# Optimization experiments

Hardware: AMD Instinct MI355X
Metric: run time of the kernel (lower is better)

The kernel has to match this reference:

```python
import jax, jax.numpy as jnp
import numpy as np

H = 512          # hidden_size
SF = 4           # scale_factor
B, S, L = 16, 2048, 2

def setup_inputs() -> dict:
    key = jax.random.key(0)
    ks = jax.random.split(key, 9)
    return {
        "hidden": jax.random.normal(ks[0], (L, B, H * SF), dtype=jnp.float32),
        "encoder_outputs": jax.random.normal(ks[1], (B, S, H * SF), dtype=jnp.float32),
        "We": jax.random.normal(ks[2], (H, H * SF), dtype=jnp.float32) * 0.02,
        "be": jax.random.normal(ks[3], (H,), dtype=jnp.float32) * 0.02,
        "Wh": jax.random.normal(ks[4], (H, H * SF), dtype=jnp.float32) * 0.02,
        "bh": jax.random.normal(ks[5], (H,), dtype=jnp.float32) * 0.02,
        "Wa": jax.random.normal(ks[6], (H, 2 * H), dtype=jnp.float32) * 0.02,
        "ba": jax.random.normal(ks[7], (H,), dtype=jnp.float32) * 0.02,
        "v": jax.random.uniform(ks[8], (1, H), dtype=jnp.float32),
    }

def reference(hidden, encoder_outputs, We, be, Wh, bh, Wa, ba, v):
    # hidden[-1]: [B, 4H] -> [B, H]
    h = hidden[-1] @ Wh.T + bh
    # encoder_outputs: [B, S, 4H] -> [B, S, H]
    eo = jnp.einsum('bsf,hf->bsh', encoder_outputs, We) + be
    # concat([h broadcast to S, eo]) @ Wa.T == h @ Wa_h.T + eo @ Wa_e.T (split concat matmul)
    Wa_h, Wa_e = Wa[:, :H], Wa[:, H:]
    energy = jnp.tanh(h[:, None, :] @ Wa_h.T + jnp.einsum('bsh,kh->bsk', eo, Wa_e) + ba)  # [B,S,H]
    scores = jnp.einsum('bsh,h->bs', energy, v[0])           # [B,S]
    attn_weights = jax.nn.softmax(scores, axis=1)            # [B,S]
    context_vector = jnp.einsum('bs,bsh->bh', attn_weights, eo)  # [B,H]
    return (context_vector, attn_weights)
```

## Files before the change

kernel.cpp:

```cpp
#include <hip/hip_runtime.h>
#include <math.h>

#define HH 512
#define FF 2048
#define BB 16
#define SS 2048
#define MM 32768

using f32x4 = __attribute__((ext_vector_type(4))) float;
using s16x8 = __attribute__((ext_vector_type(8))) short;

struct __align__(8)  US4 { unsigned short x, y, z, w; };
struct __align__(16) US8 { unsigned short s[8]; };

__device__ __forceinline__ unsigned short f2bf(float f) {
  unsigned int u = __builtin_bit_cast(unsigned int, f);
  u += 0x7fffu + ((u >> 16) & 1u);
  return (unsigned short)(u >> 16);
}
__device__ __forceinline__ float bf2f(unsigned short u) {
  unsigned int x = ((unsigned int)u) << 16;
  return __builtin_bit_cast(float, x);
}
__device__ __forceinline__ void gload_lds16(const void* g, void* l) {
  __builtin_amdgcn_global_load_lds(
      (const __attribute__((address_space(1))) unsigned int*)g,
      (__attribute__((address_space(3))) unsigned int*)l, 16, 0, 0);
}

__global__ void k_conv(const float* __restrict__ We, const float* __restrict__ Wa,
                       unsigned short* __restrict__ OWe, unsigned short* __restrict__ OWa) {
  int bid = blockIdx.x, t = threadIdx.x;
  if (bid < 1024) {
    int idx = bid * 256 + t;
    f32x4 x = *(const f32x4*)(We + (size_t)idx * 4);
    US4 p{f2bf(x.x), f2bf(x.y), f2bf(x.z), f2bf(x.w)};
    *(US4*)(OWe + (size_t)idx * 4) = p;
  } else {
    int idx = (bid - 1024) * 256 + t;
    int k = idx >> 7, h4 = idx & 127;
    f32x4 x = *(const f32x4*)(Wa + (size_t)k * 1024 + 512 + h4 * 4);
    US4 p{f2bf(x.x), f2bf(x.y), f2bf(x.z), f2bf(x.w)};
    *(US4*)(OWa + (size_t)idx * 4) = p;
  }
}

__global__ void k_h(const float* __restrict__ hidden, const float* __restrict__ Wh,
                    const float* __restrict__ bh, float* __restrict__ h_ws) {
  int t = threadIdx.x, lane = t & 63, wid = t >> 6;
  int out = blockIdx.x * 4 + wid;
  int b = out >> 9, j = out & 511;
  const float* hr = hidden + (1) * BB * FF + b * FF;
  const float* wr = Wh + (size_t)j * FF;
  float a = 0.f;
#pragma unroll
  for (int i = 0; i < 8; ++i) {
    int o = i * 256 + lane * 4;
    f32x4 x = *(const f32x4*)(hr + o);
    f32x4 y = *(const f32x4*)(wr + o);
    a += x.x * y.x + x.y * y.y + x.z * y.z + x.w * y.w;
  }
#pragma unroll
  for (int m = 32; m; m >>= 1) a += __shfl_xor(a, m);
  if (lane == 0) h_ws[out] = a + bh[j];
}

__global__ void k_bb(const float* __restrict__ h_ws, const float* __restrict__ Wa,
                     const float* __restrict__ ba, float* __restrict__ bb_ws) {
  int t = threadIdx.x, lane = t & 63, wid = t >> 6;
  int out = blockIdx.x * 4 + wid;
  int b = out >> 9, k = out & 511;
  const float* hr = h_ws + b * HH;
  const float* wa = Wa + (size_t)k * 1024;
  float a = 0.f;
#pragma unroll
  for (int i = 0; i < 2; ++i) {
    int o = i * 256 + lane * 4;
    f32x4 x = *(const f32x4*)(hr + o);
    f32x4 y = *(const f32x4*)(wa + o);
    a += x.x * y.x + x.y * y.y + x.z * y.z + x.w * y.w;
  }
#pragma unroll
  for (int m = 32; m; m >>= 1) a += __shfl_xor(a, m);
  if (lane == 0) bb_ws[out] = a + ba[k];
}

__global__ __launch_bounds__(512, 4) void k_gemm1f(
    const float* __restrict__ enc, const unsigned short* __restrict__ Web,
    const float* __restrict__ be, const unsigned short* __restrict__ Waeb,
    const float* __restrict__ bbw, const float* __restrict__ vv,
    unsigned short* __restrict__ eo, float* __restrict__ sp) {
  __shared__ unsigned short smem[36864];
  unsigned short* As = smem;
  unsigned short* Bs = smem + 4096;
  const int t = threadIdx.x, lane = t & 63, wid = t >> 6;
  const int m0 = blockIdx.x * 64;
  const float* enc_m0 = enc + (size_t)m0 * FF;
  f32x4 acc[4][4] = {};

  f32x4 areg[2];
#pragma unroll
  for (int i = 0; i < 2; ++i) {
    int idx = i * 512 + t, row = idx >> 4, c4 = idx & 15;
    areg[i] = *(const f32x4*)(enc_m0 + (size_t)row * FF + c4 * 4);
  }

#pragma unroll 1
  for (int kt = 0; kt < FF; kt += 64) {
#pragma unroll
    for (int i = 0; i < 8; ++i) {
      int idx = i * 512 + t, row = idx >> 3, c = idx & 7, sc = c ^ (row & 7);
      gload_lds16(Web + (size_t)row * FF + kt + sc * 8, Bs + idx * 8);
    }
#pragma unroll
    for (int i = 0; i < 2; ++i) {
      int idx = i * 512 + t, row = idx >> 4, c4 = idx & 15;
      f32x4 x = areg[i];
      US4 p{f2bf(x.x), f2bf(x.y), f2bf(x.z), f2bf(x.w)};
      int byte = row * 128 + ((c4 * 8) ^ ((row & 7) << 4));
      *(US4*)((char*)As + byte) = p;
    }
    {
      int ktn = (kt + 64 < FF) ? kt + 64 : 0;
#pragma unroll
      for (int i = 0; i < 2; ++i) {
        int idx = i * 512 + t, row = idx >> 4, c4 = idx & 15;
        areg[i] = *(const f32x4*)(enc_m0 + (size_t)row * FF + ktn + c4 * 4);
      }
    }
    __syncthreads();
#pragma unroll
    for (int ks = 0; ks < 2; ++ks) {
      s16x8 af[4], bfr[4];
#pragma unroll
      for (int mi = 0; mi < 4; ++mi) {
        int row = mi * 16 + (lane & 15);
        int byte = row * 128 + (((ks * 64) + (lane >> 4) * 16) ^ ((row & 7) << 4));
        af[mi] = *(const s16x8*)((const char*)As + byte);
      }
#pragma unroll
      for (int ni = 0; ni < 4; ++ni) {
        int row = wid * 64 + ni * 16 + (lane & 15);
        int byte = row * 128 + (((ks * 64) + (lane >> 4) * 16) ^ ((row & 7) << 4));
        bfr[ni] = *(const s16x8*)((const char*)Bs + byte);
      }
#pragma unroll
      for (int mi = 0; mi < 4; ++mi)
#pragma unroll
        for (int ni = 0; ni < 4; ++ni)
          acc[mi][ni] = __builtin_amdgcn_mfma_f32_16x16x32_bf16(af[mi], bfr[ni], acc[mi][ni], 0, 0, 0);
    }
    __syncthreads();
  }

  unsigned short* Cs = smem + 4096;
#pragma unroll
  for (int ni = 0; ni < 4; ++ni) {
    int col = wid * 64 + ni * 16 + (lane & 15);
    float bev = be[col];
#pragma unroll
    for (int mi = 0; mi < 4; ++mi)
#pragma unroll
      for (int j = 0; j < 4; ++j) {
        int row = mi * 16 + (lane >> 4) * 4 + j;
        int byte = row * 1024 + ((col * 2) ^ ((row & 7) << 4));
        *(unsigned short*)((char*)Cs + byte) = f2bf(acc[mi][ni][j] + bev);
      }
  }
  __syncthreads();

#pragma unroll
  for (int i = 0; i < 8; ++i) {
    int idx = i * 512 + t, row = idx >> 6, c = idx & 63;
    int byte = row * 1024 + ((c * 16) ^ ((row & 7) << 4));
    *(US8*)(eo + (size_t)(m0 + row) * HH + c * 8) = *(const US8*)((const char*)Cs + byte);
  }

  f32x4 acc2[4][4] = {};
#pragma unroll 1
  for (int kt2 = 0; kt2 < HH; kt2 += 64) {
#pragma unroll
    for (int ks = 0; ks < 2; ++ks) {
      int k2 = kt2 + ks * 32 + (lane >> 4) * 8;
      s16x8 af[4], bfr[4];
#pragma unroll
      for (int mi = 0; mi < 4; ++mi) {
        int row = mi * 16 + (lane & 15);
        int byte = row * 1024 + ((k2 * 2) ^ ((row & 7) << 4));
        af[mi] = *(const s16x8*)((const char*)Cs + byte);
      }
#pragma unroll
      for (int ni = 0; ni < 4; ++ni) {
        int nrow = wid * 64 + ni * 16 + (lane & 15);
        bfr[ni] = *(const s16x8*)(Waeb + (size_t)nrow * HH + k2);
      }
#pragma unroll
      for (int mi = 0; mi < 4; ++mi)
#pragma unroll
        for (int ni = 0; ni < 4; ++ni)
          acc2[mi][ni] = __builtin_amdgcn_mfma_f32_16x16x32_bf16(af[mi], bfr[ni], acc2[mi][ni], 0, 0, 0);
    }
  }

  const int b = m0 >> 11;
  float vcol[4], bcol[4];
#pragma unroll
  for (int ni = 0; ni < 4; ++ni) {
    int col = wid * 64 + ni * 16 + (lane & 15);
    vcol[ni] = vv[col];
    bcol[ni] = bbw[b * HH + col];
  }
  float ps[4][4];
#pragma unroll
  for (int mi = 0; mi < 4; ++mi)
#pragma unroll
    for (int j = 0; j < 4; ++j) {
      float s = 0.f;
#pragma unroll
      for (int ni = 0; ni < 4; ++ni)
        s += tanhf(acc2[mi][ni][j] + bcol[ni]) * vcol[ni];
      ps[mi][j] = s;
    }
#pragma unroll
  for (int m = 1; m < 16; m <<= 1)
#pragma unroll
    for (int mi = 0; mi < 4; ++mi)
#pragma unroll
      for (int j = 0; j < 4; ++j) ps[mi][j] += __shfl_xor(ps[mi][j], m);
  float* red = (float*)smem;
  if ((lane & 15) == 0) {
#pragma unroll
    for (int mi = 0; mi < 4; ++mi)
#pragma unroll
      for (int j = 0; j < 4; ++j)
        red[wid * 64 + mi * 16 + (lane >> 4) * 4 + j] = ps[mi][j];
  }
  __syncthreads();
  if (t < 64) {
    float s = 0.f;
#pragma unroll
    for (int w = 0; w < 8; ++w) s += red[w * 64 + t];
    sp[m0 + t] = s;
  }
}

__global__ void k_softmax(const float* __restrict__ sp, float* __restrict__ attn) {
  const int b = blockIdx.x, t = threadIdx.x, lane = t & 63, wid = t >> 6;
  __shared__ float red[4];
  float vals[8], lmax = -3.0e38f;
#pragma unroll
  for (int i = 0; i < 8; ++i) {
    float x = sp[b * SS + t + i * 256];
    vals[i] = x;
    lmax = fmaxf(lmax, x);
  }
#pragma unroll
  for (int m = 32; m; m >>= 1) lmax = fmaxf(lmax, __shfl_xor(lmax, m));
  if (lane == 0) red[wid] = lmax;
  __syncthreads();
  lmax = fmaxf(fmaxf(red[0], red[1]), fmaxf(red[2], red[3]));
  __syncthreads();
  float lsum = 0.f;
#pragma unroll
  for (int i = 0; i < 8; ++i) {
    vals[i] = __expf(vals[i] - lmax);
    lsum += vals[i];
  }
#pragma unroll
  for (int m = 32; m; m >>= 1) lsum += __shfl_xor(lsum, m);
  if (lane == 0) red[wid] = lsum;
  __syncthreads();
  float inv = 1.0f / (red[0] + red[1] + red[2] + red[3]);
#pragma unroll
  for (int i = 0; i < 8; ++i) attn[b * SS + t + i * 256] = vals[i] * inv;
}

__global__ __launch_bounds__(512) void k_ctx1(const unsigned short* __restrict__ eo,
                                              const float* __restrict__ attn,
                                              float* __restrict__ cp) {
  __shared__ float red[8][512];
  const int b = blockIdx.x >> 4, ch = blockIdx.x & 15, t = threadIdx.x;
  const int tg = t & 63, sg = t >> 6;
  const float* aw = attn + b * SS + ch * 128;
  float acc[8] = {};
#pragma unroll 4
  for (int i = 0; i < 16; ++i) {
    int s = sg + i * 8;
    float w = aw[s];
    US8 vv8 = *(const US8*)(eo + (size_t)(b * SS + ch * 128 + s) * HH + tg * 8);
#pragma unroll
    for (int j = 0; j < 8; ++j) acc[j] += w * bf2f(vv8.s[j]);
  }
#pragma unroll
  for (int j = 0; j < 8; ++j) red[sg][tg * 8 + j] = acc[j];
  __syncthreads();
  float a = 0.f;
#pragma unroll
  for (int g = 0; g < 8; ++g) a += red[g][t];
  cp[(size_t)blockIdx.x * HH + t] = a;
}

__global__ void k_ctx2(const float* __restrict__ cp, float* __restrict__ ctx) {
  const int b = blockIdx.x, h = threadIdx.x;
  float a = 0.f;
#pragma unroll
  for (int c = 0; c < 16; ++c) a += cp[(size_t)(b * 16 + c) * HH + h];
  ctx[b * HH + h] = a;
}

extern "C" void kernel_launch(void* const* d_in, const int* in_sizes, int n_in,
                              void* d_out, int out_size, void* d_ws, size_t ws_size,
                              hipStream_t stream) {
  (void)in_sizes; (void)n_in; (void)out_size; (void)ws_size;
  const float* hidden = (const float*)d_in[0];
  const float* enc    = (const float*)d_in[1];
  const float* We     = (const float*)d_in[2];
  const float* be     = (const float*)d_in[3];
  const float* Wh     = (const float*)d_in[4];
  const float* bh     = (const float*)d_in[5];
  const float* Wa     = (const float*)d_in[6];
  const float* ba     = (const float*)d_in[7];
  const float* v      = (const float*)d_in[8];

  float* out  = (float*)d_out;
  float* ctx  = out;
  float* attn = out + BB * HH;

  char* ws = (char*)d_ws;
  unsigned short* Web  = (unsigned short*)ws;  ws += (size_t)HH * FF * 2;
  unsigned short* Waeb = (unsigned short*)ws;  ws += (size_t)HH * HH * 2;
  float* h_ws  = (float*)ws;                   ws += (size_t)BB * HH * 4;
  float* bb_ws = (float*)ws;                   ws += (size_t)BB * HH * 4;
  unsigned short* eo = (unsigned short*)ws;    ws += (size_t)MM * HH * 2;
  float* sp = (float*)ws;                      ws += (size_t)MM * 4;
  float* cp = (float*)ws;                      ws += (size_t)BB * 16 * HH * 4;

  k_conv<<<1280, 256, 0, stream>>>(We, Wa, Web, Waeb);
  k_h<<<2048, 256, 0, stream>>>(hidden, Wh, bh, h_ws);
  k_bb<<<2048, 256, 0, stream>>>(h_ws, Wa, ba, bb_ws);
  k_gemm1f<<<512, 512, 0, stream>>>(enc, Web, be, Waeb, bb_ws, v, eo, sp);
  k_softmax<<<16, 256, 0, stream>>>(sp, attn);
  k_ctx1<<<256, 512, 0, stream>>>(eo, attn, cp);
  k_ctx2<<<16, 512, 0, stream>>>(cp, ctx);
}
```

Before: 168.8 us.

## Double-buffer LDS tiles in encoder GEMM with k-step of 32 and MFMA-native layout

Restructures the main encoder projection GEMM loop into a two-stage ping-pong pipeline over LDS buffers with a K-step of 32. The next A and B tiles are staged into the alternate buffer while MFMAs consume the current one, so only one barrier per step is needed instead of two. The LDS layout is changed so fragments are stored in the order the MFMA operands are read, which removes the XOR swizzle addressing. The cost is a smaller K-step per barrier, a different global access pattern for the B loads, and reliance on the new layout being free of bank conflicts.

```diff
diff --git a/kernel.cpp b/kernel.cpp
--- a/kernel.cpp
+++ b/kernel.cpp
@@ -85,73 +85,86 @@
   if (lane == 0) bb_ws[out] = a + ba[k];
 }
 
+template<int CUR, bool STAGE, bool LOADA>
+__device__ __forceinline__ void step2(
+    const float* enc_m0, const unsigned short* Web, unsigned short* smem,
+    int kB, int kA, int t, int lane, int wid,
+    const f32x4& aWr, f32x4& aLd, f32x4 (&acc)[4][4],
+    int rowA, int k0A, const int* bRow, const int* bKb) {
+  char* base = (char*)smem;
+  char* AsC = base + CUR * 4096;
+  char* AsN = base + (CUR ^ 1) * 4096;
+  char* BsC = base + 8192 + CUR * 32768;
+  char* BsN = base + 8192 + (CUR ^ 1) * 32768;
+  if (LOADA)
+    aLd = *(const f32x4*)(enc_m0 + (size_t)rowA * FF + kA + k0A);
+  if (STAGE) {
+#pragma unroll
+    for (int i = 0; i < 4; ++i) {
+      int idx = i * 512 + t;
+      gload_lds16(Web + (size_t)bRow[i] * FF + kB + bKb[i] * 8, BsN + idx * 16);
+    }
+    US4 p{f2bf(aWr.x), f2bf(aWr.y), f2bf(aWr.z), f2bf(aWr.w)};
+    *(US4*)(AsN + t * 8) = p;
+  }
+  s16x8 af[4], bfr[4];
+#pragma unroll
+  for (int mi = 0; mi < 4; ++mi)
+    af[mi] = *(const s16x8*)(AsC + (((lane >> 4) * 4 + mi) << 8) + ((lane & 15) << 4));
+#pragma unroll
+  for (int ni = 0; ni < 4; ++ni)
+    bfr[ni] = *(const s16x8*)(BsC + (((lane >> 4) * 32 + wid * 4 + ni) << 8) + ((lane & 15) << 4));
+#pragma unroll
+  for (int mi = 0; mi < 4; ++mi)
+#pragma unroll
+    for (int ni = 0; ni < 4; ++ni)
+      acc[mi][ni] = __builtin_amdgcn_mfma_f32_16x16x32_bf16(af[mi], bfr[ni], acc[mi][ni], 0, 0, 0);
+  __syncthreads();
+}
+
 __global__ __launch_bounds__(512, 4) void k_gemm1f(
     const float* __restrict__ enc, const unsigned short* __restrict__ Web,
     const float* __restrict__ be, const unsigned short* __restrict__ Waeb,
     const float* __restrict__ bbw, const float* __restrict__ vv,
     unsigned short* __restrict__ eo, float* __restrict__ sp) {
   __shared__ unsigned short smem[36864];
-  unsigned short* As = smem;
-  unsigned short* Bs = smem + 4096;
   const int t = threadIdx.x, lane = t & 63, wid = t >> 6;
   const int m0 = blockIdx.x * 64;
   const float* enc_m0 = enc + (size_t)m0 * FF;
   f32x4 acc[4][4] = {};
 
-  f32x4 areg[2];
-#pragma unroll
-  for (int i = 0; i < 2; ++i) {
-    int idx = i * 512 + t, row = idx >> 4, c4 = idx & 15;
-    areg[i] = *(const f32x4*)(enc_m0 + (size_t)row * FF + c4 * 4);
-  }
-
+  const int rowA = ((t >> 5) & 3) * 16 + ((t >> 1) & 15);
+  const int k0A  = (t >> 7) * 8 + (t & 1) * 4;
+  int bRow[4], bKb[4];
+#pragma unroll
+  for (int i = 0; i < 4; ++i) {
+    int idx = i * 512 + t;
+    bRow[i] = ((idx >> 4) & 31) * 16 + (idx & 15);
+    bKb[i]  = idx >> 9;
+  }
+
+  f32x4 a0 = *(const f32x4*)(enc_m0 + (size_t)rowA * FF + 0 + k0A);
+#pragma unroll
+  for (int i = 0; i < 4; ++i) {
+    int idx = i * 512 + t;
+    gload_lds16(Web + (size_t)bRow[i] * FF + 0 + bKb[i] * 8, (char*)smem + 8192 + idx * 16);
+  }
+  f32x4 a1 = *(const f32x4*)(enc_m0 + (size_t)rowA * FF + 32 + k0A);
+  {
+    US4 p{f2bf(a0.x), f2bf(a0.y), f2bf(a0.z), f2bf(a0.w)};
+    *(US4*)((char*)smem + t * 8) = p;
+  }
+  __syncthreads();
+
+  int kB = 32, kA = 64;
 #pragma unroll 1
-  for (int kt = 0; kt < FF; kt += 64) {
-#pragma unroll
-    for (int i = 0; i < 8; ++i) {
-      int idx = i * 512 + t, row = idx >> 3, c = idx & 7, sc = c ^ (row & 7);
-      gload_lds16(Web + (size_t)row * FF + kt + sc * 8, Bs + idx * 8);
-    }
-#pragma unroll
-    for (int i = 0; i < 2; ++i) {
-      int idx = i * 512 + t, row = idx >> 4, c4 = idx & 15;
-      f32x4 x = areg[i];
-      US4 p{f2bf(x.x), f2bf(x.y), f2bf(x.z), f2bf(x.w)};
-      int byte = row * 128 + ((c4 * 8) ^ ((row & 7) << 4));
-      *(US4*)((char*)As + byte) = p;
-    }
-    {
-      int ktn = (kt + 64 < FF) ? kt + 64 : 0;
-#pragma unroll
-      for (int i = 0; i < 2; ++i) {
-        int idx = i * 512 + t, row = idx >> 4, c4 = idx & 15;
-        areg[i] = *(const f32x4*)(enc_m0 + (size_t)row * FF + ktn + c4 * 4);
-      }
-    }
-    __syncthreads();
-#pragma unroll
-    for (int ks = 0; ks < 2; ++ks) {
-      s16x8 af[4], bfr[4];
-#pragma unroll
-      for (int mi = 0; mi < 4; ++mi) {
-        int row = mi * 16 + (lane & 15);
-        int byte = row * 128 + (((ks * 64) + (lane >> 4) * 16) ^ ((row & 7) << 4));
-        af[mi] = *(const s16x8*)((const char*)As + byte);
-      }
-#pragma unroll
-      for (int ni = 0; ni < 4; ++ni) {
-        int row = wid * 64 + ni * 16 + (lane & 15);
-        int byte = row * 128 + (((ks * 64) + (lane >> 4) * 16) ^ ((row & 7) << 4));
-        bfr[ni] = *(const s16x8*)((const char*)Bs + byte);
-      }
-#pragma unroll
-      for (int mi = 0; mi < 4; ++mi)
-#pragma unroll
-        for (int ni = 0; ni < 4; ++ni)
-          acc[mi][ni] = __builtin_amdgcn_mfma_f32_16x16x32_bf16(af[mi], bfr[ni], acc[mi][ni], 0, 0, 0);
-    }
-    __syncthreads();
-  }
+  for (int tt = 0; tt < 31; ++tt) {
+    step2<0, true, true>(enc_m0, Web, smem, kB, kA, t, lane, wid, a1, a0, acc, rowA, k0A, bRow, bKb);
+    step2<1, true, true>(enc_m0, Web, smem, kB + 32, kA + 32, t, lane, wid, a0, a1, acc, rowA, k0A, bRow, bKb);
+    kB += 64; kA += 64;
+  }
+  step2<0, true, false>(enc_m0, Web, smem, 2016, 0, t, lane, wid, a1, a0, acc, rowA, k0A, bRow, bKb);
+  step2<1, false, false>(enc_m0, Web, smem, 0, 0, t, lane, wid, a0, a1, acc, rowA, k0A, bRow, bKb);
 
   unsigned short* Cs = smem + 4096;
 #pragma unroll
```

New measurement: 304.5 us. +80.5%, slower.

## Double-buffer A tile in LDS and load W_e fragments directly from global

Applied to the files above, without the earlier changes.

Restructures the main GEMM loop of k_gemm1f. The bf16 activation tile now goes into a double-buffered LDS layout that matches the MFMA fragment order, so there is one barrier per k-step instead of two. The W_e B-operand tiles are no longer staged through LDS with global_load_lds; each wave reads its bf16 fragments straight from global memory, relying on L2/cache reuse across blocks. The A prefetch runs two steps ahead in registers. This removes the LDS staging and half the syncs, at the risk of higher global/L2 traffic and load latency on the B operand. The shared array also grows to 80 KB, which may limit how many blocks fit per CU.

```diff
diff --git a/kernel.cpp b/kernel.cpp
--- a/kernel.cpp
+++ b/kernel.cpp
@@ -21,11 +21,6 @@
 __device__ __forceinline__ float bf2f(unsigned short u) {
   unsigned int x = ((unsigned int)u) << 16;
   return __builtin_bit_cast(float, x);
-}
-__device__ __forceinline__ void gload_lds16(const void* g, void* l) {
-  __builtin_amdgcn_global_load_lds(
-      (const __attribute__((address_space(1))) unsigned int*)g,
-      (__attribute__((address_space(3))) unsigned int*)l, 16, 0, 0);
 }
 
 __global__ void k_conv(const float* __restrict__ We, const float* __restrict__ Wa,
@@ -85,75 +80,83 @@
   if (lane == 0) bb_ws[out] = a + ba[k];
 }
 
+template<int CUR, bool PREF, bool WRITE>
+__device__ __forceinline__ void stepG(
+    const float* enc_m0, const unsigned short* Web, char* smem,
+    int kt, int lane, int wid, int sRow, int sKb, int sDst,
+    f32x4& wA0, f32x4& wA1, f32x4& lA0, f32x4& lA1, f32x4 (&acc)[4][4]) {
+  char* AsC = smem + CUR * 8192;
+  char* AsN = smem + (CUR ^ 1) * 8192;
+  if (PREF) {
+    const float* p = enc_m0 + (size_t)sRow * FF + (kt + 128) + sKb * 8;
+    lA0 = *(const f32x4*)p;
+    lA1 = *(const f32x4*)(p + 4);
+  }
+#pragma unroll
+  for (int ks = 0; ks < 2; ++ks) {
+    s16x8 af[4], bfr[4];
+#pragma unroll
+    for (int ni = 0; ni < 4; ++ni) {
+      int nrow = wid * 64 + ni * 16 + (lane & 15);
+      bfr[ni] = *(const s16x8*)(Web + (size_t)nrow * FF + kt + ks * 32 + (lane >> 4) * 8);
+    }
+#pragma unroll
+    for (int mi = 0; mi < 4; ++mi)
+      af[mi] = *(const s16x8*)(AsC + ((ks * 4 + (lane >> 4)) * 4 + mi) * 256 + (lane & 15) * 16);
+#pragma unroll
+    for (int mi = 0; mi < 4; ++mi)
+#pragma unroll
+      for (int ni = 0; ni < 4; ++ni)
+        acc[mi][ni] = __builtin_amdgcn_mfma_f32_16x16x32_bf16(af[mi], bfr[ni], acc[mi][ni], 0, 0, 0);
+  }
+  if (WRITE) {
+    US8 o{f2bf(wA0.x), f2bf(wA0.y), f2bf(wA0.z), f2bf(wA0.w),
+          f2bf(wA1.x), f2bf(wA1.y), f2bf(wA1.z), f2bf(wA1.w)};
+    *(US8*)(AsN + sDst) = o;
+  }
+  __syncthreads();
+}
+
 __global__ __launch_bounds__(512, 4) void k_gemm1f(
     const float* __restrict__ enc, const unsigned short* __restrict__ Web,
     const float* __restrict__ be, const unsigned short* __restrict__ Waeb,
     const float* __restrict__ bbw, const float* __restrict__ vv,
     unsigned short* __restrict__ eo, float* __restrict__ sp) {
-  __shared__ unsigned short smem[36864];
-  unsigned short* As = smem;
-  unsigned short* Bs = smem + 4096;
+  __shared__ char smem[81920];
   const int t = threadIdx.x, lane = t & 63, wid = t >> 6;
   const int m0 = blockIdx.x * 64;
   const float* enc_m0 = enc + (size_t)m0 * FF;
   f32x4 acc[4][4] = {};
 
-  f32x4 areg[2];
-#pragma unroll
-  for (int i = 0; i < 2; ++i) {
-    int idx = i * 512 + t, row = idx >> 4, c4 = idx & 15;
-    areg[i] = *(const f32x4*)(enc_m0 + (size_t)row * FF + c4 * 4);
-  }
-
+  const int sRow = t & 63;
+  const int sKb  = t >> 6;
+  const int sDst = (sKb * 4 + (sRow >> 4)) * 256 + (sRow & 15) * 16;
+
+  f32x4 aX0, aX1, aY0, aY1;
+  {
+    const float* p = enc_m0 + (size_t)sRow * FF + sKb * 8;
+    aX0 = *(const f32x4*)p;
+    aX1 = *(const f32x4*)(p + 4);
+    US8 o{f2bf(aX0.x), f2bf(aX0.y), f2bf(aX0.z), f2bf(aX0.w),
+          f2bf(aX1.x), f2bf(aX1.y), f2bf(aX1.z), f2bf(aX1.w)};
+    *(US8*)(smem + sDst) = o;
+    const float* q = enc_m0 + (size_t)sRow * FF + 64 + sKb * 8;
+    aX0 = *(const f32x4*)q;
+    aX1 = *(const f32x4*)(q + 4);
+  }
+  __syncthreads();
+
+  int kt = 0;
 #pragma unroll 1
-  for (int kt = 0; kt < FF; kt += 64) {
-#pragma unroll
-    for (int i = 0; i < 8; ++i) {
-      int idx = i * 512 + t, row = idx >> 3, c = idx & 7, sc = c ^ (row & 7);
-      gload_lds16(Web + (size_t)row * FF + kt + sc * 8, Bs + idx * 8);
-    }
-#pragma unroll
-    for (int i = 0; i < 2; ++i) {
-      int idx = i * 512 + t, row = idx >> 4, c4 = idx & 15;
-      f32x4 x = areg[i];
-      US4 p{f2bf(x.x), f2bf(x.y), f2bf(x.z), f2bf(x.w)};
-      int byte = row * 128 + ((c4 * 8) ^ ((row & 7) << 4));
-      *(US4*)((char*)As + byte) = p;
-    }
-    {
-      int ktn = (kt + 64 < FF) ? kt + 64 : 0;
-#pragma unroll
-      for (int i = 0; i < 2; ++i) {
-        int idx = i * 512 + t, row = idx >> 4, c4 = idx & 15;
-        areg[i] = *(const f32x4*)(enc_m0 + (size_t)row * FF + ktn + c4 * 4);
-      }
-    }
-    __syncthreads();
-#pragma unroll
-    for (int ks = 0; ks < 2; ++ks) {
-      s16x8 af[4], bfr[4];
-#pragma unroll
-      for (int mi = 0; mi < 4; ++mi) {
-        int row = mi * 16 + (lane & 15);
-        int byte = row * 128 + (((ks * 64) + (lane >> 4) * 16) ^ ((row & 7) << 4));
-        af[mi] = *(const s16x8*)((const char*)As + byte);
-      }
-#pragma unroll
-      for (int ni = 0; ni < 4; ++ni) {
-        int row = wid * 64 + ni * 16 + (lane & 15);
-        int byte = row * 128 + (((ks * 64) + (lane >> 4) * 16) ^ ((row & 7) << 4));
-        bfr[ni] = *(const s16x8*)((const char*)Bs + byte);
-      }
-#pragma unroll
-      for (int mi = 0; mi < 4; ++mi)
-#pragma unroll
-        for (int ni = 0; ni < 4; ++ni)
-          acc[mi][ni] = __builtin_amdgcn_mfma_f32_16x16x32_bf16(af[mi], bfr[ni], acc[mi][ni], 0, 0, 0);
-    }
-    __syncthreads();
-  }
-
-  unsigned short* Cs = smem + 4096;
+  for (int i = 0; i < 15; ++i) {
+    stepG<0, true, true>(enc_m0, Web, smem, kt, lane, wid, sRow, sKb, sDst, aX0, aX1, aY0, aY1, acc);
+    stepG<1, true, true>(enc_m0, Web, smem, kt + 64, lane, wid, sRow, sKb, sDst, aY0, aY1, aX0, aX1, acc);
+    kt += 128;
+  }
+  stepG<0, false, true>(enc_m0, Web, smem, 1920, lane, wid, sRow, sKb, sDst, aX0, aX1, aY0, aY1, acc);
+  stepG<1, false, false>(enc_m0, Web, smem, 1984, lane, wid, sRow, sKb, sDst, aY0, aY1, aX0, aX1, acc);
+
+  unsigned short* Cs = (unsigned short*)(smem + 16384);
 #pragma unroll
   for (int ni = 0; ni < 4; ++ni) {
     int col = wid * 64 + ni * 16 + (lane & 15);
```

New measurement: 251.9 us. +49.3%, slower.
